# Kernel tuning notes

Measured on AMD Instinct MI355X. Metric: run time of the kernel, lower is better.

## Reference

```python
import jax, jax.numpy as jnp
import numpy as np

N_NODES = 50000
N_EDGES = 800000
IN_DIM = 128
HID = 128
N_GRAPHS = 256
N_CLASSES = 2
ALPHA = 0.2  # leaky relu slope
EPS_BN = 1e-5


def setup_inputs() -> dict:
    key = jax.random.key(0)
    ks = jax.random.split(key, 24)
    adjacency = jax.random.randint(ks[0], (2, N_EDGES), 0, N_NODES, dtype=jnp.int32)
    input_feature = jax.random.normal(ks[1], (N_NODES, IN_DIM), dtype=jnp.float32)
    graph_indicator = jnp.sort(jax.random.randint(ks[2], (N_NODES,), 0, N_GRAPHS, dtype=jnp.int32))
    labels = jax.random.randint(ks[3], (N_GRAPHS,), 0, N_CLASSES, dtype=jnp.int64)
    s = 0.05
    params = {
        'W1': jax.random.normal(ks[4], (IN_DIM, HID), jnp.float32) * s,
        'a1': jax.random.normal(ks[5], (2 * HID,), jnp.float32) * s,
        'bn2_g': jnp.ones((HID,), jnp.float32),
        'bn2_b': jnp.zeros((HID,), jnp.float32),
        'W2': jax.random.normal(ks[6], (HID, HID), jnp.float32) * s,
        'a2': jax.random.normal(ks[7], (2 * HID,), jnp.float32) * s,
        'bn3_g': jnp.ones((HID,), jnp.float32),
        'bn3_b': jnp.zeros((HID,), jnp.float32),
        'W3': jax.random.normal(ks[8], (HID, HID), jnp.float32) * s,
        'a3': jax.random.normal(ks[9], (2 * HID,), jnp.float32) * s,
        'fc1_w': jax.random.normal(ks[10], (HID, 2 * HID), jnp.float32) * s,
        'fc1_b': jnp.zeros((2 * HID,), jnp.float32),
        'fc2_w': jax.random.normal(ks[11], (2 * HID, HID), jnp.float32) * s,
        'fc2_b': jnp.zeros((HID,), jnp.float32),
        'fc3_w': jax.random.normal(ks[12], (HID, N_CLASSES), jnp.float32) * s,
        'fc3_b': jnp.zeros((N_CLASSES,), jnp.float32),
    }
    return dict(adjacency=adjacency, input_feature=input_feature,
                graph_indicator=graph_indicator, labels=labels, **params)


def _batchnorm(x, g, b):
    # training-mode BatchNorm1d over node dim (biased variance)
    mu = jnp.mean(x, axis=0)
    var = jnp.mean((x - mu) ** 2, axis=0)
    return (x - mu) * jax.lax.rsqrt(var + EPS_BN) * g + b


def _sp_gat(x, src, dst, W, a):
    # pyGAT SpGraphAttentionLayer (dropout disabled / eval mode)
    h = x @ W                                # [N, F]
    F = h.shape[1]
    e_src = h @ a[:F]                        # [N]
    e_dst = h @ a[F:]                        # [N]
    e = e_src[src] + e_dst[dst]              # [E]
    ee = jnp.exp(-jax.nn.leaky_relu(e, ALPHA))
    rowsum = jax.ops.segment_sum(ee, src, num_segments=N_NODES)          # [N]
    num = jax.ops.segment_sum(ee[:, None] * h[dst], src, num_segments=N_NODES)  # [N, F]
    h_prime = num / (rowsum[:, None] + 1e-16)
    return jax.nn.elu(h_prime)


def reference(adjacency, input_feature, graph_indicator, labels,
              W1, a1, bn2_g, bn2_b, W2, a2, bn3_g, bn3_b, W3, a3,
              fc1_w, fc1_b, fc2_w, fc2_b, fc3_w, fc3_b):
    src, dst = adjacency[0], adjacency[1]
    # bn1 output is discarded in the original forward
    x = _sp_gat(input_feature, src, dst, W1, a1)
    x = _batchnorm(x, bn2_g, bn2_b)
    x = _sp_gat(x, src, dst, W2, a2)
    x = _batchnorm(x, bn3_g, bn3_b)
    x = _sp_gat(x, src, dst, W3, a3)
    # pooling_sum_4tensor: per-graph sum pooling
    pooled = jax.ops.segment_sum(x, graph_indicator, num_segments=N_GRAPHS)  # [G, F]
    x = jax.nn.relu(pooled @ fc1_w + fc1_b)
    x = jax.nn.relu(x @ fc2_w + fc2_b)
    logits = x @ fc3_w + fc3_b
    return logits
```

## Files before the change

### kernel.cpp

```cpp
#include <hip/hip_runtime.h>
#include <hip/hip_bf16.h>

#define N_NODES 50000
#define N_EDGES 800000
#define FD 128
#define N_GRAPHS 256
#define NPART 6250

typedef unsigned short u16;
typedef short bf16x8 __attribute__((ext_vector_type(8)));
typedef float f32x4 __attribute__((ext_vector_type(4)));

__device__ __forceinline__ u16 f2bf(float v) {
    __hip_bfloat16 h = __float2bfloat16(v);
    union { __hip_bfloat16 hh; u16 u; } c; c.hh = h; return c.u;
}
__device__ __forceinline__ float bf2f(u16 r) {
    return __uint_as_float(((unsigned int)r) << 16);
}
__device__ __forceinline__ float rdlane_f(float v, int l) {
    return __uint_as_float((unsigned int)__builtin_amdgcn_readlane((int)__float_as_uint(v), l));
}

__global__ __launch_bounds__(256) void count_deg_part_k(const int* __restrict__ src,
                                                        int* __restrict__ cnt, int E) {
    int part = blockIdx.x & 7;
    int lo = part * NPART, hi = lo + NPART;
    int stride = (gridDim.x >> 3) * 256;
    for (int e = (blockIdx.x >> 3) * 256 + threadIdx.x; e < E; e += stride) {
        int s = src[e];
        if (s >= lo && s < hi) atomicAdd(&cnt[s], 1);
    }
}

__global__ __launch_bounds__(256) void fill_csr_part_k(const int* __restrict__ src,
                                                       const int* __restrict__ dst,
                                                       int* __restrict__ cur,
                                                       int* __restrict__ edst, int E) {
    int part = blockIdx.x & 7;
    int lo = part * NPART, hi = lo + NPART;
    int stride = (gridDim.x >> 3) * 256;
    for (int e = (blockIdx.x >> 3) * 256 + threadIdx.x; e < E; e += stride) {
        int s = src[e];
        if (s >= lo && s < hi) {
            int p = atomicAdd(&cur[s], 1);
            edst[p] = dst[e];
        }
    }
}

__global__ __launch_bounds__(256) void scan1_k(const int* __restrict__ cnt,
                                               int* __restrict__ bsum, int M,
                                               float* __restrict__ bnbuf,
                                               float* __restrict__ pooled) {
    int i = blockIdx.x * 256 + threadIdx.x;
    int v = (i < M) ? cnt[i] : 0;
    __shared__ int l[256];
    l[threadIdx.x] = v;
    __syncthreads();
    for (int s = 128; s > 0; s >>= 1) {
        if (threadIdx.x < s) l[threadIdx.x] += l[threadIdx.x + s];
        __syncthreads();
    }
    if (threadIdx.x == 0) bsum[blockIdx.x] = l[0];
    if (blockIdx.x == 0) {
        bnbuf[threadIdx.x] = 0.f; bnbuf[threadIdx.x + 256] = 0.f;
        for (int k = threadIdx.x; k < N_GRAPHS * FD; k += 256) pooled[k] = 0.f;
    }
}

__global__ __launch_bounds__(256) void scan3_k(const int* __restrict__ cnt,
                                               const int* __restrict__ bsum,
                                               int* __restrict__ offs,
                                               int* __restrict__ cur, int M, int NB) {
    int i = blockIdx.x * 256 + threadIdx.x;
    int tid = threadIdx.x;
    __shared__ int bs[256];
    bs[tid] = (tid < NB) ? bsum[tid] : 0;
    __syncthreads();
    for (int off = 1; off < 256; off <<= 1) {
        int t = (tid >= off) ? bs[tid - off] : 0;
        __syncthreads();
        bs[tid] += t;
        __syncthreads();
    }
    int base = (blockIdx.x == 0) ? 0 : bs[blockIdx.x - 1];
    int v = (i < M) ? cnt[i] : 0;
    __shared__ int l[256];
    l[tid] = v;
    __syncthreads();
    for (int off = 1; off < 256; off <<= 1) {
        int t = (tid >= off) ? l[tid - off] : 0;
        __syncthreads();
        l[tid] += t;
        __syncthreads();
    }
    int excl = l[tid] - v + base;
    if (i < M) { offs[i] = excl; cur[i] = excl; }
    if (i == M - 1) offs[M] = excl + v;
}

__global__ __launch_bounds__(256) void gemm_mfma_k(const float* __restrict__ Xf,
                                                   const u16* __restrict__ Xb,
                                                   int use_f32,
                                                   const float* __restrict__ W,
                                                   const float* __restrict__ sums,
                                                   const float* __restrict__ sumsq,
                                                   const float* __restrict__ g,
                                                   const float* __restrict__ b,
                                                   float invN, int haveBN,
                                                   const float* __restrict__ avec,
                                                   u16* __restrict__ Hb,
                                                   float* __restrict__ es,
                                                   float* __restrict__ ed, int M) {
    __shared__ u16 As[64][136];
    __shared__ u16 Bs[128][136];
    __shared__ float cv[128];
    __shared__ float scsh[256];
    int tid = threadIdx.x;
    int row0 = blockIdx.x * 64;

    if (haveBN) {
        if (tid < 128) {
            float mu = sums[tid] * invN;
            float var = sumsq[tid] * invN - mu * mu;
            float sc = g[tid] * rsqrtf(var + 1e-5f);
            scsh[tid] = sc;
            scsh[128 + tid] = b[tid] - mu * sc;
        }
        __syncthreads();
        float cvp = 0.f;
#pragma unroll 8
        for (int i = 0; i < 64; i++) {
            int idx = i * 256 + tid;
            int k = idx >> 7;
            int n = idx & 127;
            float wv = W[idx];
            Bs[n][k] = f2bf(scsh[k] * wv);
            cvp += scsh[128 + k] * wv;
        }
        __syncthreads();
        scsh[tid] = cvp;
        __syncthreads();
        if (tid < 128) cv[tid] = scsh[tid] + scsh[tid + 128];
    } else {
#pragma unroll 8
        for (int i = 0; i < 64; i++) {
            int idx = i * 256 + tid;
            Bs[idx & 127][idx >> 7] = f2bf(W[idx]);
        }
        if (tid < 128) cv[tid] = 0.f;
    }

    {
        int r = tid >> 2, k0 = (tid & 3) * 32;
        int grow = row0 + r;
        if (grow < M) {
            if (use_f32) {
                const float4* s = (const float4*)(Xf + (size_t)grow * FD + k0);
#pragma unroll
                for (int u = 0; u < 8; u++) {
                    float4 v = s[u];
                    ushort4 o;
                    o.x = f2bf(v.x); o.y = f2bf(v.y); o.z = f2bf(v.z); o.w = f2bf(v.w);
                    *(ushort4*)&As[r][k0 + u * 4] = o;
                }
            } else {
                const uint4* s = (const uint4*)(Xb + (size_t)grow * FD + k0);
#pragma unroll
                for (int u = 0; u < 4; u++) *(uint4*)&As[r][k0 + u * 8] = s[u];
            }
        } else {
            uint4 z = make_uint4(0, 0, 0, 0);
#pragma unroll
            for (int u = 0; u < 4; u++) *(uint4*)&As[r][k0 + u * 8] = z;
        }
    }
    __syncthreads();

    int wave = tid >> 6, lane = tid & 63;
    int quad = lane >> 4, n16 = lane & 15;
    int rbase = wave * 16;
    f32x4 acc[8];
    f32x4 zz = {0.f, 0.f, 0.f, 0.f};
#pragma unroll
    for (int t = 0; t < 8; t++) acc[t] = zz;

#pragma unroll
    for (int kk = 0; kk < 128; kk += 32) {
        bf16x8 a = *(const bf16x8*)&As[rbase + n16][kk + quad * 8];
#pragma unroll
        for (int t = 0; t < 8; t++) {
            bf16x8 bb = *(const bf16x8*)&Bs[t * 16 + n16][kk + quad * 8];
            acc[t] = __builtin_amdgcn_mfma_f32_16x16x32_bf16(a, bb, acc[t], 0, 0, 0);
        }
    }

    float sas[8], sad[8];
#pragma unroll
    for (int t = 0; t < 8; t++) {
        sas[t] = avec[t * 16 + n16];
        sad[t] = avec[128 + t * 16 + n16];
    }

#pragma unroll
    for (int reg = 0; reg < 4; reg++) {
        int grow = row0 + rbase + quad * 4 + reg;
        float vals[8];
        float ps = 0.f, pd = 0.f;
#pragma unroll
        for (int t = 0; t < 8; t++) {
            float v = acc[t][reg] + cv[t * 16 + n16];
            vals[t] = v;
            ps += v * sas[t];
            pd += v * sad[t];
        }
#pragma unroll
        for (int o = 8; o > 0; o >>= 1) { ps += __shfl_xor(ps, o); pd += __shfl_xor(pd, o); }
        if (grow < M) {
            if (n16 == 0) { es[grow] = ps; ed[grow] = pd; }
#pragma unroll
            for (int t = 0; t < 8; t++)
                Hb[(size_t)grow * FD + t * 16 + n16] = f2bf(vals[t]);
        }
    }
}

__global__ __launch_bounds__(256) void agg_k(const u16* __restrict__ Hb,
                                             const float* __restrict__ es_,
                                             const float* __restrict__ ed_,
                                             const int* __restrict__ offs,
                                             const int* __restrict__ edst,
                                             u16* __restrict__ Out,
                                             const int* __restrict__ gi,
                                             float* __restrict__ pooled,
                                             int M) {
    int node = __builtin_amdgcn_readfirstlane((int)((blockIdx.x * blockDim.x + threadIdx.x) >> 6));
    int lane = threadIdx.x & 63;
    if (node >= M) return;
    int s0 = offs[node], s1 = offs[node + 1];
    float esv = es_[node];
    const unsigned int* Hrow = (const unsigned int*)Hb;
    float2 a0 = make_float2(0.f, 0.f), a1 = make_float2(0.f, 0.f);
    float2 a2 = make_float2(0.f, 0.f), a3 = make_float2(0.f, 0.f);
    float rsl = 0.f;
    for (int base = s0; base < s1; base += 64) {
        int rem = s1 - base;
        int nE = rem < 64 ? rem : 64;
        int dv = 0; float wv = 0.f;
        if (lane < nE) {
            dv = edst[base + lane];
            float ev = esv + ed_[dv];
            float lr = ev > 0.f ? ev : 0.2f * ev;
            wv = __expf(-lr);
        }
        rsl += wv;
        int j = 0;
        for (; j + 8 <= nE; j += 8) {
            int d0 = __builtin_amdgcn_readlane(dv, j + 0);
            int d1 = __builtin_amdgcn_readlane(dv, j + 1);
            int d2 = __builtin_amdgcn_readlane(dv, j + 2);
            int d3 = __builtin_amdgcn_readlane(dv, j + 3);
            int d4 = __builtin_amdgcn_readlane(dv, j + 4);
            int d5 = __builtin_amdgcn_readlane(dv, j + 5);
            int d6 = __builtin_amdgcn_readlane(dv, j + 6);
            int d7 = __builtin_amdgcn_readlane(dv, j + 7);
            float w0 = rdlane_f(wv, j + 0);
            float w1 = rdlane_f(wv, j + 1);
            float w2 = rdlane_f(wv, j + 2);
            float w3 = rdlane_f(wv, j + 3);
            float w4 = rdlane_f(wv, j + 4);
            float w5 = rdlane_f(wv, j + 5);
            float w6 = rdlane_f(wv, j + 6);
            float w7 = rdlane_f(wv, j + 7);
            unsigned int r0 = Hrow[(size_t)d0 * 64 + lane];
            unsigned int r1 = Hrow[(size_t)d1 * 64 + lane];
            unsigned int r2 = Hrow[(size_t)d2 * 64 + lane];
            unsigned int r3 = Hrow[(size_t)d3 * 64 + lane];
            unsigned int r4 = Hrow[(size_t)d4 * 64 + lane];
            unsigned int r5 = Hrow[(size_t)d5 * 64 + lane];
            unsigned int r6 = Hrow[(size_t)d6 * 64 + lane];
            unsigned int r7 = Hrow[(size_t)d7 * 64 + lane];
            a0.x += w0 * __uint_as_float(r0 << 16);
            a0.y += w0 * __uint_as_float(r0 & 0xffff0000u);
            a1.x += w1 * __uint_as_float(r1 << 16);
            a1.y += w1 * __uint_as_float(r1 & 0xffff0000u);
            a2.x += w2 * __uint_as_float(r2 << 16);
            a2.y += w2 * __uint_as_float(r2 & 0xffff0000u);
            a3.x += w3 * __uint_as_float(r3 << 16);
            a3.y += w3 * __uint_as_float(r3 & 0xffff0000u);
            a0.x += w4 * __uint_as_float(r4 << 16);
            a0.y += w4 * __uint_as_float(r4 & 0xffff0000u);
            a1.x += w5 * __uint_as_float(r5 << 16);
            a1.y += w5 * __uint_as_float(r5 & 0xffff0000u);
            a2.x += w6 * __uint_as_float(r6 << 16);
            a2.y += w6 * __uint_as_float(r6 & 0xffff0000u);
            a3.x += w7 * __uint_as_float(r7 << 16);
            a3.y += w7 * __uint_as_float(r7 & 0xffff0000u);
        }
        for (; j < nE; j++) {
            int d = __builtin_amdgcn_readlane(dv, j);
            float wj = rdlane_f(wv, j);
            unsigned int r = Hrow[(size_t)d * 64 + lane];
            if (j & 1) {
                a1.x += wj * __uint_as_float(r << 16);
                a1.y += wj * __uint_as_float(r & 0xffff0000u);
            } else {
                a0.x += wj * __uint_as_float(r << 16);
                a0.y += wj * __uint_as_float(r & 0xffff0000u);
            }
        }
    }
    float rs = rsl;
#pragma unroll
    for (int o = 32; o > 0; o >>= 1) rs += __shfl_xor(rs, o);
    float inv = 1.f / (rs + 1e-16f);
    float vx = (a0.x + a1.x + a2.x + a3.x) * inv;
    float vy = (a0.y + a1.y + a2.y + a3.y) * inv;
    vx = vx > 0.f ? vx : (__expf(vx) - 1.f);
    vy = vy > 0.f ? vy : (__expf(vy) - 1.f);
    if (pooled) {
        int gg = __builtin_amdgcn_readfirstlane(gi[node]);
        atomicAdd(&pooled[(size_t)gg * FD + 2 * lane], vx);
        atomicAdd(&pooled[(size_t)gg * FD + 2 * lane + 1], vy);
    } else {
        unsigned int pk = ((unsigned int)f2bf(vy) << 16) | f2bf(vx);
        ((unsigned int*)Out)[(size_t)node * 64 + lane] = pk;
    }
}

__global__ void bnstats_b_k(const u16* __restrict__ Xb, float* __restrict__ sums,
                            float* __restrict__ sumsq, int M) {
    int f = threadIdx.x & 127;
    int half = threadIdx.x >> 7;
    float s1 = 0.f, s2 = 0.f;
    for (int r = blockIdx.x * 2 + half; r < M; r += gridDim.x * 2) {
        float v = bf2f(Xb[(size_t)r * FD + f]);
        s1 += v; s2 += v * v;
    }
    __shared__ float l1[256], l2[256];
    l1[threadIdx.x] = s1; l2[threadIdx.x] = s2;
    __syncthreads();
    if (half == 0) {
        atomicAdd(&sums[f], l1[f] + l1[f + 128]);
        atomicAdd(&sumsq[f], l2[f] + l2[f + 128]);
    }
}

__global__ __launch_bounds__(256) void mlp_k(const float* __restrict__ pooled,
                                             const float* __restrict__ fc1w, const float* __restrict__ fc1b,
                                             const float* __restrict__ fc2w, const float* __restrict__ fc2b,
                                             const float* __restrict__ fc3w, const float* __restrict__ fc3b,
                                             float* __restrict__ out) {
    int g = blockIdx.x, j = threadIdx.x;
    __shared__ float x[128], t1[256], t2[128], p0[128], p1[128];
    if (j < 128) x[j] = pooled[(size_t)g * FD + j];
    __syncthreads();
    float s = fc1b[j];
    for (int k = 0; k < 128; k++) s += x[k] * fc1w[(size_t)k * 256 + j];
    t1[j] = fmaxf(s, 0.f);
    __syncthreads();
    if (j < 128) {
        float s2 = fc2b[j];
        for (int k = 0; k < 256; k++) s2 += t1[k] * fc2w[(size_t)k * 128 + j];
        t2[j] = fmaxf(s2, 0.f);
    }
    __syncthreads();
    if (j < 128) { p0[j] = t2[j] * fc3w[j * 2]; p1[j] = t2[j] * fc3w[j * 2 + 1]; }
    __syncthreads();
    for (int s3 = 64; s3 > 0; s3 >>= 1) {
        if (j < s3) { p0[j] += p0[j + s3]; p1[j] += p1[j + s3]; }
        __syncthreads();
    }
    if (j == 0) { out[g * 2] = p0[0] + fc3b[0]; out[g * 2 + 1] = p1[0] + fc3b[1]; }
}

extern "C" void kernel_launch(void* const* d_in, const int* in_sizes, int n_in,
                              void* d_out, int out_size, void* d_ws, size_t ws_size,
                              hipStream_t stream) {
    const int*   adj  = (const int*)d_in[0];
    const float* xin  = (const float*)d_in[1];
    const int*   gi   = (const int*)d_in[2];
    const float* W1   = (const float*)d_in[4];
    const float* a1   = (const float*)d_in[5];
    const float* bn2g = (const float*)d_in[6];
    const float* bn2b = (const float*)d_in[7];
    const float* W2   = (const float*)d_in[8];
    const float* a2   = (const float*)d_in[9];
    const float* bn3g = (const float*)d_in[10];
    const float* bn3b = (const float*)d_in[11];
    const float* W3   = (const float*)d_in[12];
    const float* a3   = (const float*)d_in[13];
    const float* fc1w = (const float*)d_in[14];
    const float* fc1b = (const float*)d_in[15];
    const float* fc2w = (const float*)d_in[16];
    const float* fc2b = (const float*)d_in[17];
    const float* fc3w = (const float*)d_in[18];
    const float* fc3b = (const float*)d_in[19];
    float* out = (float*)d_out;

    const int N = N_NODES, E = N_EDGES, G = N_GRAPHS;

    u16*   Xb     = (u16*)d_ws;
    u16*   Hb     = Xb + (size_t)N * FD;
    u16*   Wt     = Hb + (size_t)N * FD;
    float* es     = (float*)(Wt + FD * FD);
    float* ed     = es + N;
    float* bnbuf  = ed + N;
    float* sumsA  = bnbuf;
    float* sumsqA = bnbuf + 128;
    float* sumsB  = bnbuf + 256;
    float* sumsqB = bnbuf + 384;
    float* cvec   = bnbuf + 512;
    float* pooled = cvec + FD;
    int*   degcnt = (int*)(pooled + (size_t)G * FD);
    int*   offs   = degcnt + N;
    int*   cur    = offs + (N + 2);
    int*   bsum   = cur + N;
    int*   edst   = bsum + 256;

    const int* srcp = adj;
    const int* dstp = adj + E;

    const int NB = (N + 255) / 256;

    hipMemsetAsync(degcnt, 0, (size_t)N * sizeof(int), stream);
    count_deg_part_k<<<8 * 392, 256, 0, stream>>>(srcp, degcnt, E);
    scan1_k<<<NB, 256, 0, stream>>>(degcnt, bsum, N, bnbuf, pooled);
    scan3_k<<<NB, 256, 0, stream>>>(degcnt, bsum, offs, cur, N, NB);
    fill_csr_part_k<<<8 * 392, 256, 0, stream>>>(srcp, dstp, cur, edst, E);

    const int gemm_grid = (N + 63) / 64;
    const int wave_grid = (N + 3) / 4;
    const float invN = 1.0f / (float)N;

    gemm_mfma_k<<<gemm_grid, 256, 0, stream>>>(xin, Xb, 1, W1,
                                               nullptr, nullptr, nullptr, nullptr, invN, 0,
                                               a1, Hb, es, ed, N);
    agg_k<<<wave_grid, 256, 0, stream>>>(Hb, es, ed, offs, edst, Xb, nullptr, nullptr, N);
    bnstats_b_k<<<256, 256, 0, stream>>>(Xb, sumsA, sumsqA, N);

    gemm_mfma_k<<<gemm_grid, 256, 0, stream>>>(nullptr, Xb, 0, W2,
                                               sumsA, sumsqA, bn2g, bn2b, invN, 1,
                                               a2, Hb, es, ed, N);
    agg_k<<<wave_grid, 256, 0, stream>>>(Hb, es, ed, offs, edst, Xb, nullptr, nullptr, N);
    bnstats_b_k<<<256, 256, 0, stream>>>(Xb, sumsB, sumsqB, N);

    gemm_mfma_k<<<gemm_grid, 256, 0, stream>>>(nullptr, Xb, 0, W3,
                                               sumsB, sumsqB, bn3g, bn3b, invN, 1,
                                               a3, Hb, es, ed, N);
    agg_k<<<wave_grid, 256, 0, stream>>>(Hb, es, ed, offs, edst, nullptr, gi, pooled, N);

    mlp_k<<<G, 256, 0, stream>>>(pooled, fc1w, fc1b, fc2w, fc2b, fc3w, fc3b, out);
}
```

Baseline: 442.2 us.

## Precompute edge attention weights in separate kernel before aggregation

Splits the per-edge attention weight computation out of the aggregation kernel into a new edge-parallel kernel that reads CSR-ordered src/dst, gathers es/ed, and writes exp(-leakyrelu) weights. The aggregation kernel then reads edge indices and weights as uniform scalar loads instead of lane-distributed loads plus readlane broadcasts and a wave reduction of rowsum. This costs an extra kernel launch per layer plus writing and rereading 800K weights and storing a CSR source array, but aims to shorten the aggregation kernel's serial dependency chain.

After: 452.3 us. +2.3%, slower.

```diff
diff --git a/kernel.cpp b/kernel.cpp
--- a/kernel.cpp
+++ b/kernel.cpp
@@ -17,9 +17,6 @@
 }
 __device__ __forceinline__ float bf2f(u16 r) {
     return __uint_as_float(((unsigned int)r) << 16);
-}
-__device__ __forceinline__ float rdlane_f(float v, int l) {
-    return __uint_as_float((unsigned int)__builtin_amdgcn_readlane((int)__float_as_uint(v), l));
 }
 
 __global__ __launch_bounds__(256) void count_deg_part_k(const int* __restrict__ src,
@@ -36,7 +33,8 @@
 __global__ __launch_bounds__(256) void fill_csr_part_k(const int* __restrict__ src,
                                                        const int* __restrict__ dst,
                                                        int* __restrict__ cur,
-                                                       int* __restrict__ edst, int E) {
+                                                       int* __restrict__ edst,
+                                                       int* __restrict__ esrc, int E) {
     int part = blockIdx.x & 7;
     int lo = part * NPART, hi = lo + NPART;
     int stride = (gridDim.x >> 3) * 256;
@@ -45,6 +43,7 @@
         if (s >= lo && s < hi) {
             int p = atomicAdd(&cur[s], 1);
             edst[p] = dst[e];
+            esrc[p] = s;
         }
     }
 }
@@ -226,9 +225,25 @@
     }
 }
 
+__global__ __launch_bounds__(256) void ew_k(const float* __restrict__ es_,
+                                            const float* __restrict__ ed_,
+                                            const int* __restrict__ esrc,
+                                            const int* __restrict__ edst,
+                                            float* __restrict__ wts) {
+    int i = blockIdx.x * 256 + threadIdx.x;
+    if (i >= N_EDGES / 4) return;
+    int4 ss = ((const int4*)esrc)[i];
+    int4 dd = ((const int4*)edst)[i];
+    float4 w;
+    { float ev = es_[ss.x] + ed_[dd.x]; float lr = ev > 0.f ? ev : 0.2f * ev; w.x = __expf(-lr); }
+    { float ev = es_[ss.y] + ed_[dd.y]; float lr = ev > 0.f ? ev : 0.2f * ev; w.y = __expf(-lr); }
+    { float ev = es_[ss.z] + ed_[dd.z]; float lr = ev > 0.f ? ev : 0.2f * ev; w.z = __expf(-lr); }
+    { float ev = es_[ss.w] + ed_[dd.w]; float lr = ev > 0.f ? ev : 0.2f * ev; w.w = __expf(-lr); }
+    ((float4*)wts)[i] = w;
+}
+
 __global__ __launch_bounds__(256) void agg_k(const u16* __restrict__ Hb,
-                                             const float* __restrict__ es_,
-                                             const float* __restrict__ ed_,
+                                             const float* __restrict__ wts,
                                              const int* __restrict__ offs,
                                              const int* __restrict__ edst,
                                              u16* __restrict__ Out,
@@ -239,81 +254,62 @@
     int lane = threadIdx.x & 63;
     if (node >= M) return;
     int s0 = offs[node], s1 = offs[node + 1];
-    float esv = es_[node];
     const unsigned int* Hrow = (const unsigned int*)Hb;
     float2 a0 = make_float2(0.f, 0.f), a1 = make_float2(0.f, 0.f);
     float2 a2 = make_float2(0.f, 0.f), a3 = make_float2(0.f, 0.f);
-    float rsl = 0.f;
-    for (int base = s0; base < s1; base += 64) {
-        int rem = s1 - base;
-        int nE = rem < 64 ? rem : 64;
-        int dv = 0; float wv = 0.f;
-        if (lane < nE) {
-            dv = edst[base + lane];
-            float ev = esv + ed_[dv];
-            float lr = ev > 0.f ? ev : 0.2f * ev;
-            wv = __expf(-lr);
-        }
-        rsl += wv;
-        int j = 0;
-        for (; j + 8 <= nE; j += 8) {
-            int d0 = __builtin_amdgcn_readlane(dv, j + 0);
-            int d1 = __builtin_amdgcn_readlane(dv, j + 1);
-            int d2 = __builtin_amdgcn_readlane(dv, j + 2);
-            int d3 = __builtin_amdgcn_readlane(dv, j + 3);
-            int d4 = __builtin_amdgcn_readlane(dv, j + 4);
-            int d5 = __builtin_amdgcn_readlane(dv, j + 5);
-            int d6 = __builtin_amdgcn_readlane(dv, j + 6);
-            int d7 = __builtin_amdgcn_readlane(dv, j + 7);
-            float w0 = rdlane_f(wv, j + 0);
-            float w1 = rdlane_f(wv, j + 1);
-            float w2 = rdlane_f(wv, j + 2);
-            float w3 = rdlane_f(wv, j + 3);
-            float w4 = rdlane_f(wv, j + 4);
-            float w5 = rdlane_f(wv, j + 5);
-            float w6 = rdlane_f(wv, j + 6);
-            float w7 = rdlane_f(wv, j + 7);
-            unsigned int r0 = Hrow[(size_t)d0 * 64 + lane];
-            unsigned int r1 = Hrow[(size_t)d1 * 64 + lane];
-            unsigned int r2 = Hrow[(size_t)d2 * 64 + lane];
-            unsigned int r3 = Hrow[(size_t)d3 * 64 + lane];
-            unsigned int r4 = Hrow[(size_t)d4 * 64 + lane];
-            unsigned int r5 = Hrow[(size_t)d5 * 64 + lane];
-            unsigned int r6 = Hrow[(size_t)d6 * 64 + lane];
-            unsigned int r7 = Hrow[(size_t)d7 * 64 + lane];
-            a0.x += w0 * __uint_as_float(r0 << 16);
-            a0.y += w0 * __uint_as_float(r0 & 0xffff0000u);
-            a1.x += w1 * __uint_as_float(r1 << 16);
-            a1.y += w1 * __uint_as_float(r1 & 0xffff0000u);
-            a2.x += w2 * __uint_as_float(r2 << 16);
-            a2.y += w2 * __uint_as_float(r2 & 0xffff0000u);
-            a3.x += w3 * __uint_as_float(r3 << 16);
-            a3.y += w3 * __uint_as_float(r3 & 0xffff0000u);
-            a0.x += w4 * __uint_as_float(r4 << 16);
-            a0.y += w4 * __uint_as_float(r4 & 0xffff0000u);
-            a1.x += w5 * __uint_as_float(r5 << 16);
-            a1.y += w5 * __uint_as_float(r5 & 0xffff0000u);
-            a2.x += w6 * __uint_as_float(r6 << 16);
-            a2.y += w6 * __uint_as_float(r6 & 0xffff0000u);
-            a3.x += w7 * __uint_as_float(r7 << 16);
-            a3.y += w7 * __uint_as_float(r7 & 0xffff0000u);
-        }
-        for (; j < nE; j++) {
-            int d = __builtin_amdgcn_readlane(dv, j);
-            float wj = rdlane_f(wv, j);
-            unsigned int r = Hrow[(size_t)d * 64 + lane];
-            if (j & 1) {
-                a1.x += wj * __uint_as_float(r << 16);
-                a1.y += wj * __uint_as_float(r & 0xffff0000u);
-            } else {
-                a0.x += wj * __uint_as_float(r << 16);
-                a0.y += wj * __uint_as_float(r & 0xffff0000u);
-            }
-        }
-    }
-    float rs = rsl;
-#pragma unroll
-    for (int o = 32; o > 0; o >>= 1) rs += __shfl_xor(rs, o);
+    float rs = 0.f;
+    int e = s0;
+    for (; e + 8 <= s1; e += 8) {
+        int d0 = __builtin_amdgcn_readfirstlane(edst[e]);
+        int d1 = __builtin_amdgcn_readfirstlane(edst[e + 1]);
+        int d2 = __builtin_amdgcn_readfirstlane(edst[e + 2]);
+        int d3 = __builtin_amdgcn_readfirstlane(edst[e + 3]);
+        int d4 = __builtin_amdgcn_readfirstlane(edst[e + 4]);
+        int d5 = __builtin_amdgcn_readfirstlane(edst[e + 5]);
+        int d6 = __builtin_amdgcn_readfirstlane(edst[e + 6]);
+        int d7 = __builtin_amdgcn_readfirstlane(edst[e + 7]);
+        float w0 = wts[e];
+        float w1 = wts[e + 1];
+        float w2 = wts[e + 2];
+        float w3 = wts[e + 3];
+        float w4 = wts[e + 4];
+        float w5 = wts[e + 5];
+        float w6 = wts[e + 6];
+        float w7 = wts[e + 7];
+        unsigned int r0 = Hrow[(size_t)d0 * 64 + lane];
+        unsigned int r1 = Hrow[(size_t)d1 * 64 + lane];
+        unsigned int r2 = Hrow[(size_t)d2 * 64 + lane];
+        unsigned int r3 = Hrow[(size_t)d3 * 64 + lane];
+        unsigned int r4 = Hrow[(size_t)d4 * 64 + lane];
+        unsigned int r5 = Hrow[(size_t)d5 * 64 + lane];
+        unsigned int r6 = Hrow[(size_t)d6 * 64 + lane];
+        unsigned int r7 = Hrow[(size_t)d7 * 64 + lane];
+        rs += w0 + w1 + w2 + w3 + w4 + w5 + w6 + w7;
+        a0.x += w0 * __uint_as_float(r0 << 16);
+        a0.y += w0 * __uint_as_float(r0 & 0xffff0000u);
+        a1.x += w1 * __uint_as_float(r1 << 16);
+        a1.y += w1 * __uint_as_float(r1 & 0xffff0000u);
+        a2.x += w2 * __uint_as_float(r2 << 16);
+        a2.y += w2 * __uint_as_float(r2 & 0xffff0000u);
+        a3.x += w3 * __uint_as_float(r3 << 16);
+        a3.y += w3 * __uint_as_float(r3 & 0xffff0000u);
+        a0.x += w4 * __uint_as_float(r4 << 16);
+        a0.y += w4 * __uint_as_float(r4 & 0xffff0000u);
+        a1.x += w5 * __uint_as_float(r5 << 16);
+        a1.y += w5 * __uint_as_float(r5 & 0xffff0000u);
+        a2.x += w6 * __uint_as_float(r6 << 16);
+        a2.y += w6 * __uint_as_float(r6 & 0xffff0000u);
+        a3.x += w7 * __uint_as_float(r7 << 16);
+        a3.y += w7 * __uint_as_float(r7 & 0xffff0000u);
+    }
+    for (; e < s1; e++) {
+        int d = __builtin_amdgcn_readfirstlane(edst[e]);
+        float wv = wts[e];
+        rs += wv;
+        unsigned int r = Hrow[(size_t)d * 64 + lane];
+        a0.x += wv * __uint_as_float(r << 16);
+        a0.y += wv * __uint_as_float(r & 0xffff0000u);
+    }
     float inv = 1.f / (rs + 1e-16f);
     float vx = (a0.x + a1.x + a2.x + a3.x) * inv;
     float vy = (a0.y + a1.y + a2.y + a3.y) * inv;
@@ -418,6 +414,8 @@
     int*   cur    = offs + (N + 2);
     int*   bsum   = cur + N;
     int*   edst   = bsum + 256;
+    int*   esrc   = edst + N_EDGES;
+    float* wts    = (float*)(esrc + N_EDGES);
 
     const int* srcp = adj;
     const int* dstp = adj + E;
@@ -428,28 +426,32 @@
     count_deg_part_k<<<8 * 392, 256, 0, stream>>>(srcp, degcnt, E);
     scan1_k<<<NB, 256, 0, stream>>>(degcnt, bsum, N, bnbuf, pooled);
     scan3_k<<<NB, 256, 0, stream>>>(degcnt, bsum, offs, cur, N, NB);
-    fill_csr_part_k<<<8 * 392, 256, 0, stream>>>(srcp, dstp, cur, edst, E);
+    fill_csr_part_k<<<8 * 392, 256, 0, stream>>>(srcp, dstp, cur, edst, esrc, E);
 
     const int gemm_grid = (N + 63) / 64;
     const int wave_grid = (N + 3) / 4;
+    const int ew_grid = (N_EDGES / 4 + 255) / 256;
     const float invN = 1.0f / (float)N;
 
     gemm_mfma_k<<<gemm_grid, 256, 0, stream>>>(xin, Xb, 1, W1,
                                                nullptr, nullptr, nullptr, nullptr, invN, 0,
                                                a1, Hb, es, ed, N);
-    agg_k<<<wave_grid, 256, 0, stream>>>(Hb, es, ed, offs, edst, Xb, nullptr, nullptr, N);
+    ew_k<<<ew_grid, 256, 0, stream>>>(es, ed, esrc, edst, wts);
+    agg_k<<<wave_grid, 256, 0, stream>>>(Hb, wts, offs, edst, Xb, nullptr, nullptr, N);
     bnstats_b_k<<<256, 256, 0, stream>>>(Xb, sumsA, sumsqA, N);
 
     gemm_mfma_k<<<gemm_grid, 256, 0, stream>>>(nullptr, Xb, 0, W2,
                                                sumsA, sumsqA, bn2g, bn2b, invN, 1,
                                                a2, Hb, es, ed, N);
-    agg_k<<<wave_grid, 256, 0, stream>>>(Hb, es, ed, offs, edst, Xb, nullptr, nullptr, N);
+    ew_k<<<ew_grid, 256, 0, stream>>>(es, ed, esrc, edst, wts);
+    agg_k<<<wave_grid, 256, 0, stream>>>(Hb, wts, offs, edst, Xb, nullptr, nullptr, N);
     bnstats_b_k<<<256, 256, 0, stream>>>(Xb, sumsB, sumsqB, N);
 
     gemm_mfma_k<<<gemm_grid, 256, 0, stream>>>(nullptr, Xb, 0, W3,
                                                sumsB, sumsqB, bn3g, bn3b, invN, 1,
                                                a3, Hb, es, ed, N);
-    agg_k<<<wave_grid, 256, 0, stream>>>(Hb, es, ed, offs, edst, nullptr, gi, pooled, N);
+    ew_k<<<ew_grid, 256, 0, stream>>>(es, ed, esrc, edst, wts);
+    agg_k<<<wave_grid, 256, 0, stream>>>(Hb, wts, offs, edst, nullptr, gi, pooled, N);
 
     mlp_k<<<G, 256, 0, stream>>>(pooled, fc1w, fc1b, fc2w, fc2b, fc3w, fc3b, out);
 }
```
